# Kernel tuning notes

Hardware: AMD Instinct MI355X
Metric: run time of the kernel (lower is better)

The kernel has to match this reference:

```python
import jax, jax.numpy as jnp
import numpy as np

NUM_USERS = 1_000_000
NUM_ITEMS = 1_000_000
F = 64
B = 16384


def setup_inputs() -> dict:
    key = jax.random.key(0)
    k1, k2, k3, k4 = jax.random.split(key, 4)
    return {
        "user_indices": jax.random.randint(k1, (B,), 0, NUM_USERS),
        "item_indices": jax.random.randint(k2, (B,), 0, NUM_ITEMS),
        "user_factors": jax.random.normal(k3, (NUM_USERS, F), dtype=jnp.float32),
        "item_factors": jax.random.normal(k4, (NUM_ITEMS, F), dtype=jnp.float32),
    }


def reference(user_indices, item_indices, user_factors, item_factors):
    # torch: mm(user_emb, item_emb.T).sum(-1)
    # == user_emb @ sum_over_batch(item_emb)  (exact linear-algebra identity)
    u = user_factors[user_indices]            # [B, F] gather
    v = item_factors[item_indices]            # [B, F] gather
    # einsum contracts both c (item batch) and f, avoiding the [B, B] intermediate
    return jnp.einsum("bf,cf->b", u, v)       # [B]
```

## Files before the change

kernel.cpp:

```cpp
#include <hip/hip_runtime.h>
#include <hip/hip_bf16.h>


#define FDIM 64
#define NB1 256
#define NB2 512
#define NTHREADS 256
#define WPB 4
#define R1 4
#define R2 2

__global__ void __launch_bounds__(NTHREADS)
mf_item_sum(const int* __restrict__ item_idx,
            const float* __restrict__ item_factors,
            float* __restrict__ s_part, int B) {
    const int lane = threadIdx.x & 63;
    const int wid  = threadIdx.x >> 6;
    const int rg   = lane >> 4;
    const int fs   = lane & 15;
    const int waveBase = (blockIdx.x * WPB + wid) * (R1 * 4);

    int idx[R1];
    #pragma unroll
    for (int r = 0; r < R1; ++r) {
        const int p = waveBase + r * 4 + rg;
        idx[r] = (p < B) ? item_idx[p] : -1;
    }

    float4 acc = make_float4(0.f, 0.f, 0.f, 0.f);
    #pragma unroll
    for (int r = 0; r < R1; ++r) {
        if (idx[r] >= 0) {
            const float4 v = *(const float4*)(item_factors + (size_t)idx[r] * FDIM + fs * 4);
            acc.x += v.x; acc.y += v.y; acc.z += v.z; acc.w += v.w;
        }
    }

    #pragma unroll
    for (int m = 16; m <= 32; m <<= 1) {
        acc.x += __shfl_xor(acc.x, m);
        acc.y += __shfl_xor(acc.y, m);
        acc.z += __shfl_xor(acc.z, m);
        acc.w += __shfl_xor(acc.w, m);
    }

    __shared__ float4 red[WPB][16];
    if (lane < 16) red[wid][fs] = acc;
    __syncthreads();
    if (threadIdx.x < 16) {
        const float4 a = red[0][threadIdx.x], b = red[1][threadIdx.x],
                     c = red[2][threadIdx.x], d = red[3][threadIdx.x];
        float4 t;
        t.x = a.x + b.x + c.x + d.x;
        t.y = a.y + b.y + c.y + d.y;
        t.z = a.z + b.z + c.z + d.z;
        t.w = a.w + b.w + c.w + d.w;
        *(float4*)(s_part + blockIdx.x * FDIM + threadIdx.x * 4) = t;
    }
}

__global__ void __launch_bounds__(NTHREADS)
mf_user_dot(const int* __restrict__ user_idx,
            const float* __restrict__ user_factors,
            const float* __restrict__ s_part,
            float* __restrict__ out, int B) {
    const int lane = threadIdx.x & 63;
    const int wid  = threadIdx.x >> 6;
    const int rg   = lane >> 4;
    const int fs   = lane & 15;

    const int waveBase = (blockIdx.x * WPB + wid) * (R2 * 4);
    int p[R2], u[R2];
    float4 uv[R2];
    #pragma unroll
    for (int r = 0; r < R2; ++r) {
        p[r] = waveBase + r * 4 + rg;
        u[r] = (p[r] < B) ? user_idx[p[r]] : -1;
    }
    #pragma unroll
    for (int r = 0; r < R2; ++r)
        uv[r] = (u[r] >= 0)
            ? *(const float4*)(user_factors + (size_t)u[r] * FDIM + fs * 4)
            : make_float4(0.f, 0.f, 0.f, 0.f);

    const float4* s_part4 = (const float4*)s_part;
    __shared__ float4 sred[16][16];
    __shared__ float4 s_lds4[16];
    {
        const int cg  = threadIdx.x >> 4;
        const int sl  = threadIdx.x & 15;
        float4 a = make_float4(0.f, 0.f, 0.f, 0.f);
        #pragma unroll
        for (int j = 0; j < 16; ++j) {
            const float4 v = s_part4[(cg * 16 + j) * 16 + sl];
            a.x += v.x; a.y += v.y; a.z += v.z; a.w += v.w;
        }
        sred[cg][sl] = a;
    }
    __syncthreads();
    if (threadIdx.x < 16) {
        float4 a = make_float4(0.f, 0.f, 0.f, 0.f);
        #pragma unroll
        for (int j = 0; j < 16; ++j) {
            const float4 v = sred[j][threadIdx.x];
            a.x += v.x; a.y += v.y; a.z += v.z; a.w += v.w;
        }
        s_lds4[threadIdx.x] = a;
    }
    __syncthreads();
    const float4 s4 = s_lds4[fs];

    #pragma unroll
    for (int r = 0; r < R2; ++r) {
        float v = uv[r].x * s4.x + uv[r].y * s4.y + uv[r].z * s4.z + uv[r].w * s4.w;
        v += __shfl_xor(v, 1);
        v += __shfl_xor(v, 2);
        v += __shfl_xor(v, 4);
        v += __shfl_xor(v, 8);
        if (fs == 0 && p[r] < B) out[p[r]] = v;
    }
}

extern "C" void kernel_launch(void* const* d_in, const int* in_sizes, int n_in,
                              void* d_out, int out_size, void* d_ws, size_t ws_size,
                              hipStream_t stream) {
    const int*   user_idx     = (const int*)d_in[0];
    const int*   item_idx     = (const int*)d_in[1];
    const float* user_factors = (const float*)d_in[2];
    const float* item_factors = (const float*)d_in[3];
    float*       out          = (float*)d_out;
    float*       s_part       = (float*)d_ws;
    const int B = in_sizes[0];

    mf_item_sum<<<NB1, NTHREADS, 0, stream>>>(item_idx, item_factors, s_part, B);
    mf_user_dot<<<NB2, NTHREADS, 0, stream>>>(user_idx, user_factors, s_part, out, B);
}
```

Before: 13.49 us.

## Pre-gather user rows in item-sum kernel into contiguous workspace buffer

The first kernel now also gathers the user factor rows and writes them to a contiguous workspace buffer, alongside the item sum. The second kernel then reads those rows with coalesced sequential loads instead of random gathers, so the random-access latency is moved into the first kernel where it overlaps with the item gather. The cost is an extra 4 MB write and 4 MB read of the staged rows, plus reliance on the workspace being large enough; if it is not, the old two-kernel path is used.

```diff
diff --git a/kernel.cpp b/kernel.cpp
--- a/kernel.cpp
+++ b/kernel.cpp
@@ -4,35 +4,43 @@
 
 #define FDIM 64
 #define NB1 256
-#define NB2 512
+#define NB2 256
 #define NTHREADS 256
 #define WPB 4
 #define R1 4
-#define R2 2
+#define R2 4
+#define S_PART_BYTES (NB1 * FDIM * 4)
 
+template <bool PREGATHER>
 __global__ void __launch_bounds__(NTHREADS)
-mf_item_sum(const int* __restrict__ item_idx,
-            const float* __restrict__ item_factors,
-            float* __restrict__ s_part, int B) {
+mf_gather_sum(const int* __restrict__ item_idx, const int* __restrict__ user_idx,
+              const float* __restrict__ item_factors, const float* __restrict__ user_factors,
+              float* __restrict__ s_part, float* __restrict__ u_g, int B) {
     const int lane = threadIdx.x & 63;
     const int wid  = threadIdx.x >> 6;
     const int rg   = lane >> 4;
     const int fs   = lane & 15;
-    const int waveBase = (blockIdx.x * WPB + wid) * (R1 * 4);
+    const int waveBase = (blockIdx.x * WPB + wid) * 16;
 
-    int idx[R1];
+    int ip[R1], up[R1];
     #pragma unroll
     for (int r = 0; r < R1; ++r) {
         const int p = waveBase + r * 4 + rg;
-        idx[r] = (p < B) ? item_idx[p] : -1;
+        ip[r] = (p < B) ? item_idx[p] : -1;
+        up[r] = (PREGATHER && p < B) ? user_idx[p] : -1;
     }
 
     float4 acc = make_float4(0.f, 0.f, 0.f, 0.f);
     #pragma unroll
     for (int r = 0; r < R1; ++r) {
-        if (idx[r] >= 0) {
-            const float4 v = *(const float4*)(item_factors + (size_t)idx[r] * FDIM + fs * 4);
+        const int p = waveBase + r * 4 + rg;
+        if (ip[r] >= 0) {
+            const float4 v = *(const float4*)(item_factors + (size_t)ip[r] * FDIM + fs * 4);
             acc.x += v.x; acc.y += v.y; acc.z += v.z; acc.w += v.w;
+        }
+        if (PREGATHER && up[r] >= 0) {
+            const float4 uvv = *(const float4*)(user_factors + (size_t)up[r] * FDIM + fs * 4);
+            *(float4*)(u_g + (size_t)p * FDIM + fs * 4) = uvv;
         }
     }
 
@@ -59,36 +67,13 @@
     }
 }
 
-__global__ void __launch_bounds__(NTHREADS)
-mf_user_dot(const int* __restrict__ user_idx,
-            const float* __restrict__ user_factors,
-            const float* __restrict__ s_part,
-            float* __restrict__ out, int B) {
-    const int lane = threadIdx.x & 63;
-    const int wid  = threadIdx.x >> 6;
-    const int rg   = lane >> 4;
-    const int fs   = lane & 15;
-
-    const int waveBase = (blockIdx.x * WPB + wid) * (R2 * 4);
-    int p[R2], u[R2];
-    float4 uv[R2];
-    #pragma unroll
-    for (int r = 0; r < R2; ++r) {
-        p[r] = waveBase + r * 4 + rg;
-        u[r] = (p[r] < B) ? user_idx[p[r]] : -1;
-    }
-    #pragma unroll
-    for (int r = 0; r < R2; ++r)
-        uv[r] = (u[r] >= 0)
-            ? *(const float4*)(user_factors + (size_t)u[r] * FDIM + fs * 4)
-            : make_float4(0.f, 0.f, 0.f, 0.f);
-
+__device__ __forceinline__ float4 reduce_s(const float* s_part, int fs) {
     const float4* s_part4 = (const float4*)s_part;
     __shared__ float4 sred[16][16];
     __shared__ float4 s_lds4[16];
     {
-        const int cg  = threadIdx.x >> 4;
-        const int sl  = threadIdx.x & 15;
+        const int cg = threadIdx.x >> 4;
+        const int sl = threadIdx.x & 15;
         float4 a = make_float4(0.f, 0.f, 0.f, 0.f);
         #pragma unroll
         for (int j = 0; j < 16; ++j) {
@@ -108,7 +93,66 @@
         s_lds4[threadIdx.x] = a;
     }
     __syncthreads();
-    const float4 s4 = s_lds4[fs];
+    return s_lds4[fs];
+}
+
+__global__ void __launch_bounds__(NTHREADS)
+mf_dot_pre(const float* __restrict__ u_g, const float* __restrict__ s_part,
+           float* __restrict__ out, int B) {
+    const int lane = threadIdx.x & 63;
+    const int wid  = threadIdx.x >> 6;
+    const int rg   = lane >> 4;
+    const int fs   = lane & 15;
+    const int waveBase = (blockIdx.x * WPB + wid) * 16;
+
+    float4 uv[R2];
+    #pragma unroll
+    for (int r = 0; r < R2; ++r) {
+        const int p = waveBase + r * 4 + rg;
+        uv[r] = (p < B)
+            ? *(const float4*)(u_g + (size_t)p * FDIM + fs * 4)
+            : make_float4(0.f, 0.f, 0.f, 0.f);
+    }
+
+    const float4 s4 = reduce_s(s_part, fs);
+
+    #pragma unroll
+    for (int r = 0; r < R2; ++r) {
+        const int p = waveBase + r * 4 + rg;
+        float v = uv[r].x * s4.x + uv[r].y * s4.y + uv[r].z * s4.z + uv[r].w * s4.w;
+        v += __shfl_xor(v, 1);
+        v += __shfl_xor(v, 2);
+        v += __shfl_xor(v, 4);
+        v += __shfl_xor(v, 8);
+        if (fs == 0 && p < B) out[p] = v;
+    }
+}
+
+__global__ void __launch_bounds__(NTHREADS)
+mf_user_dot(const int* __restrict__ user_idx,
+            const float* __restrict__ user_factors,
+            const float* __restrict__ s_part,
+            float* __restrict__ out, int B) {
+    const int lane = threadIdx.x & 63;
+    const int wid  = threadIdx.x >> 6;
+    const int rg   = lane >> 4;
+    const int fs   = lane & 15;
+    const int waveBase = (blockIdx.x * WPB + wid) * 16;
+
+    int p[R2], u[R2];
+    float4 uv[R2];
+    #pragma unroll
+    for (int r = 0; r < R2; ++r) {
+        p[r] = waveBase + r * 4 + rg;
+        u[r] = (p[r] < B) ? user_idx[p[r]] : -1;
+    }
+    #pragma unroll
+    for (int r = 0; r < R2; ++r)
+        uv[r] = (u[r] >= 0)
+            ? *(const float4*)(user_factors + (size_t)u[r] * FDIM + fs * 4)
+            : make_float4(0.f, 0.f, 0.f, 0.f);
+
+    const float4 s4 = reduce_s(s_part, fs);
 
     #pragma unroll
     for (int r = 0; r < R2; ++r) {
@@ -132,6 +176,15 @@
     float*       s_part       = (float*)d_ws;
     const int B = in_sizes[0];
 
-    mf_item_sum<<<NB1, NTHREADS, 0, stream>>>(item_idx, item_factors, s_part, B);
-    mf_user_dot<<<NB2, NTHREADS, 0, stream>>>(user_idx, user_factors, s_part, out, B);
+    const size_t need = (size_t)S_PART_BYTES + (size_t)B * FDIM * 4;
+    if (ws_size >= need) {
+        float* u_g = (float*)((char*)d_ws + S_PART_BYTES);
+        mf_gather_sum<true><<<NB1, NTHREADS, 0, stream>>>(
+            item_idx, user_idx, item_factors, user_factors, s_part, u_g, B);
+        mf_dot_pre<<<NB2, NTHREADS, 0, stream>>>(u_g, s_part, out, B);
+    } else {
+        mf_gather_sum<false><<<NB1, NTHREADS, 0, stream>>>(
+            item_idx, user_idx, item_factors, user_factors, s_part, nullptr, B);
+        mf_user_dot<<<512, NTHREADS, 0, stream>>>(user_idx, user_factors, s_part, out, B);
+    }
 }
```

After: 13.39 us. No clear change (-0.8%).
